# Performance work log

Measured on AMD Instinct MI355X. Metric: run time of the kernel, lower is better.

The kernel has to match this reference:

```python
import jax, jax.numpy as jnp
import numpy as np

SEQLEN = (512, 1024, 2048, 1536, 768, 1280, 896, 640)
HEAD_NUM = 16
HIDDEN = 1024  # head_size = 64


def setup_inputs() -> dict:
    key = jax.random.key(0)
    k1, k2 = jax.random.split(key)
    total_a = HEAD_NUM * sum(s * s for s in SEQLEN)  # packed per-seq (H, s, s) blocks
    a = jax.random.normal(k1, (total_a,), dtype=jnp.float32) * 0.02
    b = jax.random.normal(k2, (sum(SEQLEN), HIDDEN), dtype=jnp.float32)
    return {"a": a, "b": b, "seqlen": list(SEQLEN), "head_num": HEAD_NUM}


def reference(a, b, seqlen, head_num):
    """Ragged strided bmm2: per sequence i, per head h:
    C_i[:, h*hs:(h+1)*hs] = A_i[h] @ B_i[:, h*hs:(h+1)*hs].
    a packed flat as sum_i (head_num, s_i, s_i); b is (sum(s), hidden).
    """
    hidden = b.shape[1]
    hs = hidden // head_num
    outs = []
    a_off = 0
    t_off = 0
    for s in seqlen:  # static loop over ragged batch (lengths are compile-time)
        ai = jax.lax.dynamic_slice(a, (a_off,), (head_num * s * s,)).reshape(head_num, s, s)
        bi = jax.lax.dynamic_slice(b, (t_off, 0), (s, hidden)).reshape(s, head_num, hs)
        # (H, q, k) x (k, H, d) -> (q, H, d) -> (q, hidden)
        ci = jnp.einsum('hqk,khd->qhd', ai, bi).reshape(s, hidden)
        outs.append(ci)
        a_off += head_num * s * s
        t_off += s
    return jnp.concatenate(outs, axis=0)  # (sum(seqlen), hidden)
```

## Files before the change

### kernel.cpp

```cpp
#include <hip/hip_runtime.h>
#include <hip/hip_bf16.h>

typedef __attribute__((ext_vector_type(4))) float f32x4;
typedef __attribute__((ext_vector_type(8))) short bf16x8;

__device__ __forceinline__ unsigned cvt2(float lo, float hi) {
    float2 t; t.x = lo; t.y = hi;
    __hip_bfloat162 h = __float22bfloat162_rn(t);
    union { __hip_bfloat162 h; unsigned u; } c; c.h = h; return c.u;
}
__device__ __forceinline__ bf16x8 cvt8(f32x4 lo, f32x4 hi) {
    union { bf16x8 v; unsigned u[4]; } r;
    r.u[0] = cvt2(lo[0], lo[1]); r.u[1] = cvt2(lo[2], lo[3]);
    r.u[2] = cvt2(hi[0], hi[1]); r.u[3] = cvt2(hi[2], hi[3]);
    return r.v;
}

__global__ __launch_bounds__(128, 4) void bmm2_k(const float* __restrict__ a,
                                                 const float* __restrict__ b,
                                                 float* __restrict__ out) {
    const int  cumblk[9] = {0,512,896,1216,1472,1696,1888,2048,2176};
    const int  slen[8]   = {2048,1536,1280,1024,896,768,640,512};
    const long aoff[8]   = {20971520,88080384,135266304,4194304,161480704,125829120,174325760,0};
    const int  toff[8]   = {1536,3584,5888,512,7168,5120,8064,0};

    __shared__ unsigned short Bt[2][64 * 72];

    int bid = blockIdx.x;
    int i = 0;
    #pragma unroll
    for (int t = 0; t < 7; ++t) if (bid >= cumblk[t + 1]) i = t + 1;
    int rem  = bid - cumblk[i];
    int s    = slen[i];
    int nmb  = s >> 6;
    int head = rem / nmb;
    int mb   = rem - head * nmb;

    const float* A  = a + aoff[i] + (long)head * s * s + (long)mb * 64 * s;
    const float* Bp = b + (long)toff[i] * 1024 + head * 64;
    float*       Cp = out + (long)(toff[i] + mb * 64) * 1024 + head * 64;

    int tid = threadIdx.x, lane = tid & 63, wave = tid >> 6;
    int lrow = lane & 15, lgrp = lane >> 4;

    int j0 = (tid & 15) * 4;
    int kb = (tid >> 4) * 8;
    const float* bsrc = Bp + (long)kb * 1024 + j0;

    const float* ar0 = A + (long)(wave * 32 + lrow) * s + lgrp * 8;
    const float* ar1 = ar0 + (long)16 * s;

    f32x4 acc[2][4] = {};
    int NT = s >> 6;

    {
        f32x4 r[8];
        #pragma unroll
        for (int q = 0; q < 8; ++q) r[q] = *(const f32x4*)(bsrc + (long)q * 1024);
        #pragma unroll
        for (int e = 0; e < 4; ++e) {
            uint4 w;
            w.x = cvt2(r[0][e], r[1][e]); w.y = cvt2(r[2][e], r[3][e]);
            w.z = cvt2(r[4][e], r[5][e]); w.w = cvt2(r[6][e], r[7][e]);
            *(uint4*)&Bt[0][(j0 + e) * 72 + kb] = w;
        }
    }
    __syncthreads();

    for (int t = 0; t < NT; ++t) {
        int cur = t & 1, nxt = cur ^ 1;
        int k0 = t << 6;
        int kn = (t + 1 < NT) ? (k0 + 64) : 0;

        f32x4 r[8];
        #pragma unroll
        for (int q = 0; q < 8; ++q) r[q] = *(const f32x4*)(bsrc + (long)(kn + q) * 1024);

        __syncthreads();

        #pragma unroll
        for (int e = 0; e < 4; ++e) {
            uint4 w;
            w.x = cvt2(r[0][e], r[1][e]); w.y = cvt2(r[2][e], r[3][e]);
            w.z = cvt2(r[4][e], r[5][e]); w.w = cvt2(r[6][e], r[7][e]);
            *(uint4*)&Bt[nxt][(j0 + e) * 72 + kb] = w;
        }

        f32x4 a000 = *(const f32x4*)(ar0 + k0);
        f32x4 a001 = *(const f32x4*)(ar0 + k0 + 4);
        f32x4 a010 = *(const f32x4*)(ar0 + k0 + 32);
        f32x4 a011 = *(const f32x4*)(ar0 + k0 + 36);
        f32x4 a100 = *(const f32x4*)(ar1 + k0);
        f32x4 a101 = *(const f32x4*)(ar1 + k0 + 4);
        f32x4 a110 = *(const f32x4*)(ar1 + k0 + 32);
        f32x4 a111 = *(const f32x4*)(ar1 + k0 + 36);

        {
            bf16x8 af0 = cvt8(a000, a001), af1 = cvt8(a100, a101);
            bf16x8 bf[4];
            #pragma unroll
            for (int n = 0; n < 4; ++n)
                bf[n] = *(const bf16x8*)&Bt[cur][(n * 16 + lrow) * 72 + lgrp * 8];
            #pragma unroll
            for (int n = 0; n < 4; ++n) {
                acc[0][n] = __builtin_amdgcn_mfma_f32_16x16x32_bf16(af0, bf[n], acc[0][n], 0, 0, 0);
                acc[1][n] = __builtin_amdgcn_mfma_f32_16x16x32_bf16(af1, bf[n], acc[1][n], 0, 0, 0);
            }
        }
        {
            bf16x8 af2 = cvt8(a010, a011), af3 = cvt8(a110, a111);
            bf16x8 bf[4];
            #pragma unroll
            for (int n = 0; n < 4; ++n)
                bf[n] = *(const bf16x8*)&Bt[cur][(n * 16 + lrow) * 72 + 32 + lgrp * 8];
            #pragma unroll
            for (int n = 0; n < 4; ++n) {
                acc[0][n] = __builtin_amdgcn_mfma_f32_16x16x32_bf16(af2, bf[n], acc[0][n], 0, 0, 0);
                acc[1][n] = __builtin_amdgcn_mfma_f32_16x16x32_bf16(af3, bf[n], acc[1][n], 0, 0, 0);
            }
        }
    }

    #pragma unroll
    for (int mt = 0; mt < 2; ++mt)
        #pragma unroll
        for (int n = 0; n < 4; ++n)
            #pragma unroll
            for (int rr = 0; rr < 4; ++rr) {
                int q = wave * 32 + mt * 16 + lgrp * 4 + rr;
                Cp[(long)q * 1024 + n * 16 + lrow] = acc[mt][n][rr];
            }
}

extern "C" void kernel_launch(void* const* d_in, const int* in_sizes, int n_in,
                              void* d_out, int out_size, void* d_ws, size_t ws_size,
                              hipStream_t stream) {
    const float* a = (const float*)d_in[0];
    const float* b = (const float*)d_in[1];
    float* out = (float*)d_out;
    bmm2_k<<<2176, 128, 0, stream>>>(a, b, out);
}
```

Baseline: 191.6 us.

## Stage A tiles through LDS with 128-row blocks and 256 threads

The block tile grows from 64 to 128 output rows with 256 threads, which halves the grid and halves how often each B tile is reloaded and converted. A is no longer loaded per lane straight into MFMA registers. It is loaded with coalesced row-contiguous float4 loads, converted to bf16, and staged in LDS along with B, using register prefetch of the next k-tile. This aims for better coalescing of the dominant A stream and less redundant B traffic. The cost is an extra LDS round trip for A, two barriers per iteration with a single LDS buffer, and fewer blocks available for latency hiding.

Result: faster. 178.1 us (-7.1%).

```diff
diff --git a/kernel.cpp b/kernel.cpp
--- a/kernel.cpp
+++ b/kernel.cpp
@@ -3,28 +3,24 @@
 
 typedef __attribute__((ext_vector_type(4))) float f32x4;
 typedef __attribute__((ext_vector_type(8))) short bf16x8;
+typedef __attribute__((ext_vector_type(4))) short bf16x4;
 
 __device__ __forceinline__ unsigned cvt2(float lo, float hi) {
     float2 t; t.x = lo; t.y = hi;
     __hip_bfloat162 h = __float22bfloat162_rn(t);
     union { __hip_bfloat162 h; unsigned u; } c; c.h = h; return c.u;
 }
-__device__ __forceinline__ bf16x8 cvt8(f32x4 lo, f32x4 hi) {
-    union { bf16x8 v; unsigned u[4]; } r;
-    r.u[0] = cvt2(lo[0], lo[1]); r.u[1] = cvt2(lo[2], lo[3]);
-    r.u[2] = cvt2(hi[0], hi[1]); r.u[3] = cvt2(hi[2], hi[3]);
-    return r.v;
-}
 
-__global__ __launch_bounds__(128, 4) void bmm2_k(const float* __restrict__ a,
+__global__ __launch_bounds__(256, 3) void bmm2_k(const float* __restrict__ a,
                                                  const float* __restrict__ b,
                                                  float* __restrict__ out) {
-    const int  cumblk[9] = {0,512,896,1216,1472,1696,1888,2048,2176};
+    const int  cumblk[9] = {0,256,448,608,736,848,944,1024,1088};
     const int  slen[8]   = {2048,1536,1280,1024,896,768,640,512};
     const long aoff[8]   = {20971520,88080384,135266304,4194304,161480704,125829120,174325760,0};
     const int  toff[8]   = {1536,3584,5888,512,7168,5120,8064,0};
 
-    __shared__ unsigned short Bt[2][64 * 72];
+    __shared__ unsigned short As[128 * 72];
+    __shared__ unsigned short Bs[64 * 72];
 
     int bid = blockIdx.x;
     int i = 0;
@@ -32,91 +28,75 @@
     for (int t = 0; t < 7; ++t) if (bid >= cumblk[t + 1]) i = t + 1;
     int rem  = bid - cumblk[i];
     int s    = slen[i];
-    int nmb  = s >> 6;
+    int nmb  = s >> 7;
     int head = rem / nmb;
     int mb   = rem - head * nmb;
 
-    const float* A  = a + aoff[i] + (long)head * s * s + (long)mb * 64 * s;
+    const float* A  = a + aoff[i] + (long)head * s * s + (long)mb * 128 * s;
     const float* Bp = b + (long)toff[i] * 1024 + head * 64;
-    float*       Cp = out + (long)(toff[i] + mb * 64) * 1024 + head * 64;
+    float*       Cp = out + (long)(toff[i] + mb * 128) * 1024 + head * 64;
 
     int tid = threadIdx.x, lane = tid & 63, wave = tid >> 6;
     int lrow = lane & 15, lgrp = lane >> 4;
 
-    int j0 = (tid & 15) * 4;
-    int kb = (tid >> 4) * 8;
-    const float* bsrc = Bp + (long)kb * 1024 + j0;
+    int arow = tid >> 4;
+    int kf   = (tid & 15) * 4;
+    const float* Ast = A + (long)arow * s + kf;
 
-    const float* ar0 = A + (long)(wave * 32 + lrow) * s + lgrp * 8;
-    const float* ar1 = ar0 + (long)16 * s;
+    int bj0 = (tid & 15) * 4;
+    int bk0 = (tid >> 4) * 4;
+    const float* Bst = Bp + (long)bk0 * 1024 + bj0;
 
+    f32x4 rA[8], rB[4];
     f32x4 acc[2][4] = {};
     int NT = s >> 6;
 
-    {
-        f32x4 r[8];
+    #pragma unroll
+    for (int q = 0; q < 8; ++q) rA[q] = *(const f32x4*)(Ast + (long)(q * 16) * s);
+    #pragma unroll
+    for (int q = 0; q < 4; ++q) rB[q] = *(const f32x4*)(Bst + (long)q * 1024);
+
+    for (int t = 0; t < NT; ++t) {
+        __syncthreads();
+
         #pragma unroll
-        for (int q = 0; q < 8; ++q) r[q] = *(const f32x4*)(bsrc + (long)q * 1024);
+        for (int q = 0; q < 8; ++q) {
+            int r = q * 16 + arow;
+            union { bf16x4 v; unsigned u[2]; } w;
+            w.u[0] = cvt2(rA[q][0], rA[q][1]);
+            w.u[1] = cvt2(rA[q][2], rA[q][3]);
+            *(bf16x4*)&As[r * 72 + kf] = w.v;
+        }
         #pragma unroll
         for (int e = 0; e < 4; ++e) {
-            uint4 w;
-            w.x = cvt2(r[0][e], r[1][e]); w.y = cvt2(r[2][e], r[3][e]);
-            w.z = cvt2(r[4][e], r[5][e]); w.w = cvt2(r[6][e], r[7][e]);
-            *(uint4*)&Bt[0][(j0 + e) * 72 + kb] = w;
+            union { bf16x4 v; unsigned u[2]; } w;
+            w.u[0] = cvt2(rB[0][e], rB[1][e]);
+            w.u[1] = cvt2(rB[2][e], rB[3][e]);
+            *(bf16x4*)&Bs[(bj0 + e) * 72 + bk0] = w.v;
         }
-    }
-    __syncthreads();
-
-    for (int t = 0; t < NT; ++t) {
-        int cur = t & 1, nxt = cur ^ 1;
-        int k0 = t << 6;
-        int kn = (t + 1 < NT) ? (k0 + 64) : 0;
-
-        f32x4 r[8];
-        #pragma unroll
-        for (int q = 0; q < 8; ++q) r[q] = *(const f32x4*)(bsrc + (long)(kn + q) * 1024);
 
         __syncthreads();
 
-        #pragma unroll
-        for (int e = 0; e < 4; ++e) {
-            uint4 w;
-            w.x = cvt2(r[0][e], r[1][e]); w.y = cvt2(r[2][e], r[3][e]);
-            w.z = cvt2(r[4][e], r[5][e]); w.w = cvt2(r[6][e], r[7][e]);
-            *(uint4*)&Bt[nxt][(j0 + e) * 72 + kb] = w;
+        if (t + 1 < NT) {
+            int kn = (t + 1) << 6;
+            #pragma unroll
+            for (int q = 0; q < 8; ++q) rA[q] = *(const f32x4*)(Ast + (long)(q * 16) * s + kn);
+            #pragma unroll
+            for (int q = 0; q < 4; ++q) rB[q] = *(const f32x4*)(Bst + (long)(kn + q) * 1024);
         }
 
-        f32x4 a000 = *(const f32x4*)(ar0 + k0);
-        f32x4 a001 = *(const f32x4*)(ar0 + k0 + 4);
-        f32x4 a010 = *(const f32x4*)(ar0 + k0 + 32);
-        f32x4 a011 = *(const f32x4*)(ar0 + k0 + 36);
-        f32x4 a100 = *(const f32x4*)(ar1 + k0);
-        f32x4 a101 = *(const f32x4*)(ar1 + k0 + 4);
-        f32x4 a110 = *(const f32x4*)(ar1 + k0 + 32);
-        f32x4 a111 = *(const f32x4*)(ar1 + k0 + 36);
-
-        {
-            bf16x8 af0 = cvt8(a000, a001), af1 = cvt8(a100, a101);
+        #pragma unroll
+        for (int ks = 0; ks < 2; ++ks) {
+            bf16x8 af0 = *(const bf16x8*)&As[(wave * 32 + lrow) * 72 + ks * 32 + lgrp * 8];
+            bf16x8 af1 = *(const bf16x8*)&As[(wave * 32 + 16 + lrow) * 72 + ks * 32 + lgrp * 8];
             bf16x8 bf[4];
             #pragma unroll
             for (int n = 0; n < 4; ++n)
-                bf[n] = *(const bf16x8*)&Bt[cur][(n * 16 + lrow) * 72 + lgrp * 8];
+                bf[n] = *(const bf16x8*)&Bs[(n * 16 + lrow) * 72 + ks * 32 + lgrp * 8];
             #pragma unroll
             for (int n = 0; n < 4; ++n) {
                 acc[0][n] = __builtin_amdgcn_mfma_f32_16x16x32_bf16(af0, bf[n], acc[0][n], 0, 0, 0);
                 acc[1][n] = __builtin_amdgcn_mfma_f32_16x16x32_bf16(af1, bf[n], acc[1][n], 0, 0, 0);
-            }
-        }
-        {
-            bf16x8 af2 = cvt8(a010, a011), af3 = cvt8(a110, a111);
-            bf16x8 bf[4];
-            #pragma unroll
-            for (int n = 0; n < 4; ++n)
-                bf[n] = *(const bf16x8*)&Bt[cur][(n * 16 + lrow) * 72 + 32 + lgrp * 8];
-            #pragma unroll
-            for (int n = 0; n < 4; ++n) {
-                acc[0][n] = __builtin_amdgcn_mfma_f32_16x16x32_bf16(af2, bf[n], acc[0][n], 0, 0, 0);
-                acc[1][n] = __builtin_amdgcn_mfma_f32_16x16x32_bf16(af3, bf[n], acc[1][n], 0, 0, 0);
             }
         }
     }
@@ -126,9 +106,9 @@
         #pragma unroll
         for (int n = 0; n < 4; ++n)
             #pragma unroll
-            for (int rr = 0; rr < 4; ++rr) {
-                int q = wave * 32 + mt * 16 + lgrp * 4 + rr;
-                Cp[(long)q * 1024 + n * 16 + lrow] = acc[mt][n][rr];
+            for (int r = 0; r < 4; ++r) {
+                int q = wave * 32 + mt * 16 + lgrp * 4 + r;
+                Cp[(long)q * 1024 + n * 16 + lrow] = acc[mt][n][r];
             }
 }
 
@@ -138,5 +118,5 @@
     const float* a = (const float*)d_in[0];
     const float* b = (const float*)d_in[1];
     float* out = (float*)d_out;
-    bmm2_k<<<2176, 128, 0, stream>>>(a, b, out);
+    bmm2_k<<<1088, 256, 0, stream>>>(a, b, out);
 }
```
